# Kernel tuning notes

Measured on AMD Instinct MI355X. Metric: run time of the kernel, lower is better.

Reference implementation:

```python
import jax, jax.numpy as jnp
import numpy as np


def setup_inputs() -> dict:
    key = jax.random.key(0)
    k1, k2 = jax.random.split(key)
    S, H = 16384, 2048
    # scale down so the (unshifted-exp in the original) dot products stay in a
    # sane range; our reference uses a numerically stable softmax (same math).
    enc = jax.random.normal(k1, (S, H), dtype=jnp.float32) * 0.05
    dec = jax.random.normal(k2, (1, H), dtype=jnp.float32) * 0.05
    return {"encoder_hiddens": enc, "decoder_hidden": dec}


def reference(encoder_hiddens, decoder_hidden):
    # encoder_hiddens: [S, H] (stacked list of [1, H] vectors)
    # decoder_hidden:  [1, H]
    # alignment_i = exp(<enc_i, dec>); weights = alignment / sum(alignment)
    scores = jnp.einsum("sh,h->s", encoder_hiddens, decoder_hidden[0])  # [S]
    weights = jax.nn.softmax(scores)  # stable form of exp / sum(exp)
    # context = sum_i w_i * enc_i  -> [1, H]
    context = jnp.einsum("s,sh->h", weights, encoder_hiddens)[None, :]
    return context
```

## Files before the change

### kernel.cpp

```cpp
#include <hip/hip_runtime.h>

#define H        2048
#define H4       (H / 4)
#define WAVES    4
#define RPW      4
#define RPB      (WAVES * RPW)
#define ROWS_RC  64

__device__ __forceinline__ float dpp_add_step(float x, float acc, int ctrl_unused) {
    return x;
}
__device__ __forceinline__ float wave_allsum_dpp(float x) {
    int v;
    v = __builtin_amdgcn_update_dpp(0, __float_as_int(x), 0x111, 0xf, 0xf, false);
    x += __int_as_float(v);
    v = __builtin_amdgcn_update_dpp(0, __float_as_int(x), 0x112, 0xf, 0xf, false);
    x += __int_as_float(v);
    v = __builtin_amdgcn_update_dpp(0, __float_as_int(x), 0x114, 0xf, 0xf, false);
    x += __int_as_float(v);
    v = __builtin_amdgcn_update_dpp(0, __float_as_int(x), 0x118, 0xf, 0xf, false);
    x += __int_as_float(v);
    v = __builtin_amdgcn_update_dpp(0, __float_as_int(x), 0x142, 0xf, 0xf, false);
    x += __int_as_float(v);
    v = __builtin_amdgcn_update_dpp(0, __float_as_int(x), 0x143, 0xf, 0xf, false);
    x += __int_as_float(v);
    return __int_as_float(__builtin_amdgcn_readlane(__float_as_int(x), 63));
}

__global__ __launch_bounds__(256, 4) void ctx_pass1(
    const float* __restrict__ enc, const float* __restrict__ dec,
    float* __restrict__ partials, float* __restrict__ Zarr)
{
    __shared__ float red[WAVES][H];
    __shared__ float ldsz[WAVES];

    const int tid  = threadIdx.x;
    const int wave = tid >> 6;
    const int lane = tid & 63;

    {
        const float4* dec4 = (const float4*)dec;
        float4* dkl = (float4*)red[0];
        dkl[tid]       = dec4[tid];
        dkl[tid + 256] = dec4[tid + 256];
    }
    __syncthreads();

    const float4* enc4 = (const float4*)enc;
    const float4* dkl4 = ((const float4*)red[0]) + lane;

    float4 acc[8];
#pragma unroll
    for (int k = 0; k < 8; ++k) acc[k] = make_float4(0.f, 0.f, 0.f, 0.f);

    float z = 0.f;
    const int row0 = blockIdx.x * RPB + wave * RPW;
    const float4* rp = enc4 + (size_t)row0 * H4 + lane;

    float4 rb[8], rbn[8];
#pragma unroll
    for (int k = 0; k < 8; ++k) rb[k] = rp[k * 64];

#pragma unroll
    for (int r = 0; r < RPW; ++r) {
        float d = 0.f;
#pragma unroll
        for (int k = 0; k < 8; ++k) {
            const float4 dv = dkl4[k * 64];
            d += rb[k].x * dv.x + rb[k].y * dv.y +
                 rb[k].z * dv.z + rb[k].w * dv.w;
        }

        if (r + 1 < RPW) {
            const float4* rp2 = rp + (size_t)(r + 1) * H4;
#pragma unroll
            for (int k = 0; k < 8; ++k) rbn[k] = rp2[k * 64];
        }

        const float dsum = wave_allsum_dpp(d);

        const float e = expf(dsum);
        z += e;

#pragma unroll
        for (int k = 0; k < 8; ++k) {
            acc[k].x += e * rb[k].x;
            acc[k].y += e * rb[k].y;
            acc[k].z += e * rb[k].z;
            acc[k].w += e * rb[k].w;
        }

        if (r + 1 < RPW) {
#pragma unroll
            for (int k = 0; k < 8; ++k) rb[k] = rbn[k];
        }
    }

    __syncthreads();

    float4* ldsw = (float4*)red[wave];
#pragma unroll
    for (int k = 0; k < 8; ++k) ldsw[k * 64 + lane] = acc[k];
    if (lane == 0) ldsz[wave] = z;
    __syncthreads();

    const float4* l0 = (const float4*)red[0];
    const float4* l1 = (const float4*)red[1];
    const float4* l2 = (const float4*)red[2];
    const float4* l3 = (const float4*)red[3];
    float4* p4 = (float4*)(partials + (size_t)blockIdx.x * H);

#pragma unroll
    for (int half = 0; half < 2; ++half) {
        const int idx = half * 256 + tid;
        const float4 a = l0[idx], b = l1[idx], c = l2[idx], e4 = l3[idx];
        float4 s;
        s.x = (a.x + b.x) + (c.x + e4.x);
        s.y = (a.y + b.y) + (c.y + e4.y);
        s.z = (a.z + b.z) + (c.z + e4.z);
        s.w = (a.w + b.w) + (c.w + e4.w);
        p4[idx] = s;
    }
    if (tid == 0)
        Zarr[blockIdx.x] = (ldsz[0] + ldsz[1]) + (ldsz[2] + ldsz[3]);
}

__global__ void ctx_pass2(const float* __restrict__ partials,
                          float* __restrict__ s2)
{
    const int t   = threadIdx.x;
    const int cc  = blockIdx.x;
    const int rc  = blockIdx.y;
    const int col = cc * 256 + t;
    const size_t base = (size_t)rc * ROWS_RC * H + col;

    float a0 = 0.f, a1 = 0.f, a2 = 0.f, a3 = 0.f;
    for (int r = 0; r < ROWS_RC; r += 4) {
        a0 += partials[base + (size_t)(r    ) * H];
        a1 += partials[base + (size_t)(r + 1) * H];
        a2 += partials[base + (size_t)(r + 2) * H];
        a3 += partials[base + (size_t)(r + 3) * H];
    }
    s2[(size_t)rc * H + col] = (a0 + a1) + (a2 + a3);
}

__global__ void ctx_pass3(const float* __restrict__ s2,
                          const float* __restrict__ Zarr, int nb, int nrc,
                          float* __restrict__ out)
{
    __shared__ float zl[256];
    const int t = threadIdx.x;

    float zs = 0.f;
    for (int i = t; i < nb; i += 256) zs += Zarr[i];
    zl[t] = zs;
    __syncthreads();
    for (int s = 128; s > 0; s >>= 1) {
        if (t < s) zl[t] += zl[t + s];
        __syncthreads();
    }
    const float inv = 1.0f / zl[0];

    const int col = blockIdx.x * 256 + t;
    float s = 0.f;
    for (int rc = 0; rc < nrc; ++rc) s += s2[(size_t)rc * H + col];
    out[col] = s * inv;
}

extern "C" void kernel_launch(void* const* d_in, const int* in_sizes, int n_in,
                              void* d_out, int out_size, void* d_ws, size_t ws_size,
                              hipStream_t stream) {
    const float* enc = (const float*)d_in[0];
    const float* dec = (const float*)d_in[1];
    float* out = (float*)d_out;

    const int S  = in_sizes[0] / H;
    const int nb = S / RPB;
    const int nrc = nb / ROWS_RC;

    float* partials = (float*)d_ws;
    float* Zarr     = partials + (size_t)nb * H;
    float* s2       = Zarr + nb;

    ctx_pass1<<<nb, 256, 0, stream>>>(enc, dec, partials, Zarr);
    ctx_pass2<<<dim3(H / 256, nrc), 256, 0, stream>>>(partials, s2);
    ctx_pass3<<<H / 256, 256, 0, stream>>>(s2, Zarr, nb, nrc, out);
}
```

Measured before the change: 38.34 us.

## Shrink pass1 LDS with serialized wave accumulation and drop manual prefetch

Pass 1 no longer keeps a 4×H LDS reduction buffer. It uses a single H-sized combine buffer that the waves add into one after another, each step separated by a barrier. The explicit next-row register prefetch (rbn) is removed and launch bounds rise to 5 blocks per CU, with the goal of lower LDS and register pressure and higher occupancy. In exchange the block-level reduction becomes serial, with four barriers, and loads for the next row are no longer overlapped explicitly.

```diff
diff --git a/kernel.cpp b/kernel.cpp
--- a/kernel.cpp
+++ b/kernel.cpp
@@ -7,9 +7,6 @@
 #define RPB      (WAVES * RPW)
 #define ROWS_RC  64
 
-__device__ __forceinline__ float dpp_add_step(float x, float acc, int ctrl_unused) {
-    return x;
-}
 __device__ __forceinline__ float wave_allsum_dpp(float x) {
     int v;
     v = __builtin_amdgcn_update_dpp(0, __float_as_int(x), 0x111, 0xf, 0xf, false);
@@ -27,42 +24,43 @@
     return __int_as_float(__builtin_amdgcn_readlane(__float_as_int(x), 63));
 }
 
-__global__ __launch_bounds__(256, 4) void ctx_pass1(
+__global__ __launch_bounds__(256, 5) void ctx_pass1(
     const float* __restrict__ enc, const float* __restrict__ dec,
     float* __restrict__ partials, float* __restrict__ Zarr)
 {
-    __shared__ float red[WAVES][H];
-    __shared__ float ldsz[WAVES];
+    __shared__ float decl[H];
+    __shared__ float comb[H];
+    __shared__ float zb[WAVES];
 
     const int tid  = threadIdx.x;
-    const int wave = tid >> 6;
+    const int w    = tid >> 6;
     const int lane = tid & 63;
 
     {
         const float4* dec4 = (const float4*)dec;
-        float4* dkl = (float4*)red[0];
-        dkl[tid]       = dec4[tid];
-        dkl[tid + 256] = dec4[tid + 256];
+        float4* dl4 = (float4*)decl;
+        dl4[tid]       = dec4[tid];
+        dl4[tid + 256] = dec4[tid + 256];
     }
     __syncthreads();
 
     const float4* enc4 = (const float4*)enc;
-    const float4* dkl4 = ((const float4*)red[0]) + lane;
+    const float4* dkl4 = ((const float4*)decl) + lane;
 
     float4 acc[8];
 #pragma unroll
     for (int k = 0; k < 8; ++k) acc[k] = make_float4(0.f, 0.f, 0.f, 0.f);
 
     float z = 0.f;
-    const int row0 = blockIdx.x * RPB + wave * RPW;
+    const int row0 = blockIdx.x * RPB + w * RPW;
     const float4* rp = enc4 + (size_t)row0 * H4 + lane;
-
-    float4 rb[8], rbn[8];
-#pragma unroll
-    for (int k = 0; k < 8; ++k) rb[k] = rp[k * 64];
 
 #pragma unroll
     for (int r = 0; r < RPW; ++r) {
+        float4 rb[8];
+#pragma unroll
+        for (int k = 0; k < 8; ++k) rb[k] = rp[(size_t)r * H4 + k * 64];
+
         float d = 0.f;
 #pragma unroll
         for (int k = 0; k < 8; ++k) {
@@ -71,14 +69,7 @@
                  rb[k].z * dv.z + rb[k].w * dv.w;
         }
 
-        if (r + 1 < RPW) {
-            const float4* rp2 = rp + (size_t)(r + 1) * H4;
-#pragma unroll
-            for (int k = 0; k < 8; ++k) rbn[k] = rp2[k * 64];
-        }
-
         const float dsum = wave_allsum_dpp(d);
-
         const float e = expf(dsum);
         z += e;
 
@@ -89,40 +80,34 @@
             acc[k].z += e * rb[k].z;
             acc[k].w += e * rb[k].w;
         }
-
-        if (r + 1 < RPW) {
-#pragma unroll
-            for (int k = 0; k < 8; ++k) rb[k] = rbn[k];
-        }
     }
 
-    __syncthreads();
+    if (lane == 0) zb[w] = z;
+    float4* c4 = (float4*)comb;
+#pragma unroll
+    for (int ww = 0; ww < WAVES; ++ww) {
+        if (w == ww) {
+            if (ww == 0) {
+#pragma unroll
+                for (int k = 0; k < 8; ++k) c4[k * 64 + lane] = acc[k];
+            } else {
+#pragma unroll
+                for (int k = 0; k < 8; ++k) {
+                    float4 t = c4[k * 64 + lane];
+                    t.x += acc[k].x; t.y += acc[k].y;
+                    t.z += acc[k].z; t.w += acc[k].w;
+                    c4[k * 64 + lane] = t;
+                }
+            }
+        }
+        __syncthreads();
+    }
 
-    float4* ldsw = (float4*)red[wave];
-#pragma unroll
-    for (int k = 0; k < 8; ++k) ldsw[k * 64 + lane] = acc[k];
-    if (lane == 0) ldsz[wave] = z;
-    __syncthreads();
-
-    const float4* l0 = (const float4*)red[0];
-    const float4* l1 = (const float4*)red[1];
-    const float4* l2 = (const float4*)red[2];
-    const float4* l3 = (const float4*)red[3];
     float4* p4 = (float4*)(partials + (size_t)blockIdx.x * H);
-
-#pragma unroll
-    for (int half = 0; half < 2; ++half) {
-        const int idx = half * 256 + tid;
-        const float4 a = l0[idx], b = l1[idx], c = l2[idx], e4 = l3[idx];
-        float4 s;
-        s.x = (a.x + b.x) + (c.x + e4.x);
-        s.y = (a.y + b.y) + (c.y + e4.y);
-        s.z = (a.z + b.z) + (c.z + e4.z);
-        s.w = (a.w + b.w) + (c.w + e4.w);
-        p4[idx] = s;
-    }
+    p4[tid]       = c4[tid];
+    p4[tid + 256] = c4[tid + 256];
     if (tid == 0)
-        Zarr[blockIdx.x] = (ldsz[0] + ldsz[1]) + (ldsz[2] + ldsz[3]);
+        Zarr[blockIdx.x] = (zb[0] + zb[1]) + (zb[2] + zb[3]);
 }
 
 __global__ void ctx_pass2(const float* __restrict__ partials,
```

Result: slower. 63.02 us (+64.4%).
